# Optimization experiments

Hardware: AMD Instinct MI355X
Metric: run time of the kernel (lower is better)

Reference implementation:

```python
import jax, jax.numpy as jnp
import numpy as np

EPS = 1e-10
N_NODES = 100000
OUT_CH = 128
N_EDGES = 625000


def setup_inputs() -> dict:
    key = jax.random.key(0)
    k_emb, k_eidx, k_enorm, k_lw, k_sw = jax.random.split(key, 5)
    emb = jax.random.normal(k_emb, (N_NODES, OUT_CH), dtype=jnp.float32) * 0.02
    edge_index = jax.random.randint(k_eidx, (2, N_EDGES), 0, N_NODES, dtype=jnp.int64)
    edge_norm = jax.random.uniform(k_enorm, (N_EDGES,), dtype=jnp.float32)
    scale = 1.0 / np.sqrt(OUT_CH)
    loc_w = jax.random.normal(k_lw, (OUT_CH, OUT_CH), dtype=jnp.float32) * scale
    loc_b = jnp.zeros((OUT_CH,), dtype=jnp.float32)
    std_w = jax.random.normal(k_sw, (OUT_CH, OUT_CH), dtype=jnp.float32) * scale
    std_b = jnp.zeros((OUT_CH,), dtype=jnp.float32)
    return {"emb": emb, "edge_index": edge_index, "edge_norm": edge_norm,
            "loc_w": loc_w, "loc_b": loc_b, "std_w": std_w, "std_b": std_b}


def reference(emb, edge_index, edge_norm, loc_w, loc_b, std_w, std_b):
    """GraphEncoder (GraphConv gather-scale-scatter + Linear loc/std) followed by
    GraphDecoder dot-product logits on the same edge list. Eval mode: z = loc."""
    sidx = edge_index[0]
    tidx = edge_index[1]
    # GraphConv: message = x[sidx] * enorm ; scatter_add into target nodes
    message = emb[sidx] * edge_norm[:, None]               # [E, C]
    ptr = jax.ops.segment_sum(message, tidx, num_segments=emb.shape[0])  # [N, C]
    # Encoder heads (torch Linear: x @ W.T + b)
    loc = ptr @ loc_w.T + loc_b                            # [N, C]
    std = jax.nn.softplus(ptr @ std_w.T + std_b) + EPS     # [N, C]
    z = loc  # eval-mode embedding
    # GraphDecoder: Bernoulli logits per edge
    logits = jnp.sum(z[sidx] * z[tidx], axis=1)            # [E]
    return loc, std, logits
```

## Files before the change

### kernel.cpp

```cpp
#include <hip/hip_runtime.h>

#define N_NODES 100000
#define OUT_CH  128
#define N_EDGES 625000

typedef short short8 __attribute__((ext_vector_type(8)));
typedef float f32x4  __attribute__((ext_vector_type(4)));
typedef float f32x2  __attribute__((ext_vector_type(2)));

__device__ inline short f32_bf16(float f) {
    union { float f; unsigned u; } c{f};
    unsigned r = 0x7FFFu + ((c.u >> 16) & 1u);
    return (short)((c.u + r) >> 16);
}
__device__ inline float bf16_f32(short s) {
    union { unsigned u; float f; } c;
    c.u = ((unsigned)(unsigned short)s) << 16;
    return c.f;
}
__device__ inline unsigned pack_bf16x2(float lo, float hi) {
    return (unsigned)(unsigned short)f32_bf16(lo) |
           ((unsigned)(unsigned short)f32_bf16(hi) << 16);
}
__device__ inline float sp_fast(float x) {
    float e = __expf(-fabsf(x));
    return fmaxf(x, 0.f) + __logf(1.f + e);
}

#if defined(__has_builtin)
#if __has_builtin(__builtin_amdgcn_cvt_pk_f32_fp8) && __has_builtin(__builtin_amdgcn_cvt_pk_fp8_f32)
#define HWFP8 1
#endif
#endif
#ifndef HWFP8
#define HWFP8 0
#endif

__device__ inline unsigned f32_fp8_manual(float f) {
    union { float fl; unsigned u; } c{f};
    unsigned s = (c.u >> 31) << 7;
    float af = fabsf(f);
    if (!(af < 448.f)) return s | 0x7E;
    if (af < 0.015625f) {
        unsigned q = (unsigned)__float2int_rn(af * 512.f);
        return s | q;
    }
    unsigned u = c.u;
    u += 0x7FFFF + ((u >> 20) & 1);
    int e = (int)((u >> 23) & 255) - 127;
    if (e > 8) return s | 0x7E;
    return s | (((unsigned)(e + 7)) << 3) | ((u >> 20) & 7);
}
__device__ inline float fp8_f32_manual(unsigned b) {
    unsigned s = (b >> 7) & 1, e = (b >> 3) & 15, m = b & 7;
    if (e) { union { unsigned u; float f; } c{(s << 31) | ((e + 120) << 23) | (m << 20)}; return c.f; }
    float v = (float)m * 0.001953125f;
    return s ? -v : v;
}

template <bool HI>
__device__ inline f32x2 fp8x2_f32(unsigned v) {
#if HWFP8
    return __builtin_amdgcn_cvt_pk_f32_fp8((int)v, HI);
#else
    unsigned sh = HI ? 16 : 0;
    f32x2 r;
    r.x = fp8_f32_manual((v >> sh) & 0xff);
    r.y = fp8_f32_manual((v >> (sh + 8)) & 0xff);
    return r;
#endif
}
template <bool HI>
__device__ inline unsigned fp8_pack2(float a, float b, unsigned old) {
#if HWFP8
    return (unsigned)__builtin_amdgcn_cvt_pk_fp8_f32(a, b, (int)old, HI);
#else
    unsigned v = f32_fp8_manual(a) | (f32_fp8_manual(b) << 8);
    return HI ? ((old & 0x0000ffffu) | (v << 16)) : ((old & 0xffff0000u) | v);
#endif
}

#define NBB 16
#define NBE 6250
#define NBH 2442
__global__ void prep_all(const float* __restrict__ lw, const float* __restrict__ sw,
                         short8* __restrict__ B, const float4* __restrict__ emb,
                         uint2* __restrict__ embf8, const int* __restrict__ ei,
                         int* __restrict__ counts, int use_fp8) {
    int bid = blockIdx.x, tid = threadIdx.x;
    if (bid < NBB) {
        int g = bid * 256 + tid;
        int lane = g & 63, nt = (g >> 6) & 15, ks = g >> 10;
        int c = nt * 16 + (lane & 15);
        int k = ks * 32 + (lane >> 4) * 8;
        const float* src = (c < OUT_CH) ? (lw + c * OUT_CH + k)
                                        : (sw + (c - OUT_CH) * OUT_CH + k);
        short8 o;
#pragma unroll
        for (int j = 0; j < 8; ++j) o[j] = f32_bf16(src[j]);
        B[(ks * 16 + nt) * 64 + lane] = o;
    } else if (bid < NBB + NBE) {
        if (!use_fp8) return;
        int i = (bid - NBB) * 256 + tid;
        float4 a = emb[2 * i], b = emb[2 * i + 1];
        unsigned lo = fp8_pack2<false>(a.x * 64.f, a.y * 64.f, 0u);
        lo = fp8_pack2<true>(a.z * 64.f, a.w * 64.f, lo);
        unsigned hi = fp8_pack2<false>(b.x * 64.f, b.y * 64.f, 0u);
        hi = fp8_pack2<true>(b.z * 64.f, b.w * 64.f, hi);
        uint2 o; o.x = lo; o.y = hi;
        embf8[i] = o;
    } else {
        int e = (bid - NBB - NBE) * 256 + tid;
        if (e < N_EDGES) atomicAdd(&counts[ei[N_EDGES + e]], 1);
    }
}

__global__ void scan1_k(const int* __restrict__ counts, int* __restrict__ offsets,
                        int* __restrict__ partials, int* __restrict__ cursors) {
    __shared__ int wsum[16];
    int tid = threadIdx.x, lane = tid & 63, wid = tid >> 6;
    int e = blockIdx.x * 1024 + tid;
    int v = (e < N_NODES) ? counts[e] : 0;
    int incl = v;
#pragma unroll
    for (int d = 1; d < 64; d <<= 1) {
        int t = __shfl_up(incl, d);
        if (lane >= d) incl += t;
    }
    if (lane == 63) wsum[wid] = incl;
    __syncthreads();
    if (wid == 0) {
        int w = (lane < 16) ? wsum[lane] : 0;
        int wi = w;
#pragma unroll
        for (int d = 1; d < 16; d <<= 1) {
            int t = __shfl_up(wi, d);
            if (lane >= d) wi += t;
        }
        if (lane < 16) wsum[lane] = wi - w;
        if (lane == 15) partials[blockIdx.x] = wi;
    }
    __syncthreads();
    int excl = incl - v + wsum[wid];
    if (e < N_NODES) { offsets[e] = excl; cursors[e] = excl; }
}

__global__ void scan2_k(int* __restrict__ partials, int nb) {
    int lane = threadIdx.x;
    int i0 = 2 * lane, i1 = 2 * lane + 1;
    int v0 = (i0 < nb) ? partials[i0] : 0;
    int v1 = (i1 < nb) ? partials[i1] : 0;
    int s = v0 + v1;
    int incl = s;
#pragma unroll
    for (int d = 1; d < 64; d <<= 1) {
        int t = __shfl_up(incl, d);
        if (lane >= d) incl += t;
    }
    int excl = incl - s;
    if (i0 < nb) partials[i0] = excl;
    if (i1 < nb) partials[i1] = excl + v0;
}

__global__ void reorder_k(const int* __restrict__ ei, const float* __restrict__ en,
                          const int* __restrict__ partials, int* __restrict__ cursors,
                          int2* __restrict__ pairs, int2* __restrict__ et, float nscale) {
    int e = blockIdx.x * blockDim.x + threadIdx.x;
    if (e >= N_EDGES) return;
    int t = ei[N_EDGES + e];
    int pos = partials[t >> 10] + atomicAdd(&cursors[t], 1);
    int2 p; p.x = ei[e]; p.y = __float_as_int(en[e] * nscale);
    pairs[pos] = p;
    int2 q; q.x = e; q.y = t;
    et[pos] = q;
}

__global__ void gather_fp8_k(const unsigned short* __restrict__ embf8,
                             const int* __restrict__ offsets,
                             const int* __restrict__ partials,
                             const int2* __restrict__ pairs,
                             unsigned* __restrict__ ptrb) {
    int g = blockIdx.x * blockDim.x + threadIdx.x;
    int node = __builtin_amdgcn_readfirstlane(g >> 6);
    int lane = threadIdx.x & 63;
    if (node >= N_NODES) return;
    int beg = offsets[node] + partials[node >> 10];
    int end = (node == N_NODES - 1) ? N_EDGES
              : offsets[node + 1] + partials[(node + 1) >> 10];
    float ax = 0.f, ay = 0.f;
    int j = beg;
    for (; j + 4 <= end; j += 4) {
        int2 p0 = pairs[j], p1 = pairs[j + 1], p2 = pairs[j + 2], p3 = pairs[j + 3];
        unsigned v0 = embf8[(size_t)p0.x * 64 + lane];
        unsigned v1 = embf8[(size_t)p1.x * 64 + lane];
        unsigned v2 = embf8[(size_t)p2.x * 64 + lane];
        unsigned v3 = embf8[(size_t)p3.x * 64 + lane];
        float n0f = __int_as_float(p0.y), n1f = __int_as_float(p1.y);
        float n2f = __int_as_float(p2.y), n3f = __int_as_float(p3.y);
        f32x2 d0 = fp8x2_f32<false>(v0), d1 = fp8x2_f32<false>(v1);
        f32x2 d2 = fp8x2_f32<false>(v2), d3 = fp8x2_f32<false>(v3);
        ax += d0.x * n0f + d1.x * n1f + d2.x * n2f + d3.x * n3f;
        ay += d0.y * n0f + d1.y * n1f + d2.y * n2f + d3.y * n3f;
    }
    for (; j < end; ++j) {
        int2 p = pairs[j];
        float nm = __int_as_float(p.y);
        f32x2 d = fp8x2_f32<false>(embf8[(size_t)p.x * 64 + lane]);
        ax += d.x * nm; ay += d.y * nm;
    }
    ptrb[(size_t)node * 64 + lane] = pack_bf16x2(ax, ay);
}

__global__ void gather_f32_k(const float* __restrict__ emb,
                             const int* __restrict__ offsets,
                             const int* __restrict__ partials,
                             const int2* __restrict__ pairs,
                             unsigned* __restrict__ ptrb) {
    int g = blockIdx.x * blockDim.x + threadIdx.x;
    int node = __builtin_amdgcn_readfirstlane(g >> 6);
    int lane = threadIdx.x & 63;
    if (node >= N_NODES) return;
    int beg = offsets[node] + partials[node >> 10];
    int end = (node == N_NODES - 1) ? N_EDGES
              : offsets[node + 1] + partials[(node + 1) >> 10];
    float ax = 0.f, ay = 0.f;
    const float2* base = (const float2*)emb;
    int j = beg;
    for (; j + 4 <= end; j += 4) {
        int2 p0 = pairs[j], p1 = pairs[j + 1], p2 = pairs[j + 2], p3 = pairs[j + 3];
        float2 v0 = base[(size_t)p0.x * 64 + lane];
        float2 v1 = base[(size_t)p1.x * 64 + lane];
        float2 v2 = base[(size_t)p2.x * 64 + lane];
        float2 v3 = base[(size_t)p3.x * 64 + lane];
        float n0f = __int_as_float(p0.y), n1f = __int_as_float(p1.y);
        float n2f = __int_as_float(p2.y), n3f = __int_as_float(p3.y);
        ax += v0.x * n0f + v1.x * n1f + v2.x * n2f + v3.x * n3f;
        ay += v0.y * n0f + v1.y * n1f + v2.y * n2f + v3.y * n3f;
    }
    for (; j < end; ++j) {
        int2 p = pairs[j];
        float nm = __int_as_float(p.y);
        float2 v = base[(size_t)p.x * 64 + lane];
        ax += v.x * nm; ay += v.y * nm;
    }
    ptrb[(size_t)node * 64 + lane] = pack_bf16x2(ax, ay);
}

__global__ __launch_bounds__(256) void gemm_k(const short* __restrict__ P,
                                              float* __restrict__ out,
                                              const short8* __restrict__ B,
                                              const float* __restrict__ lb,
                                              const float* __restrict__ sb,
                                              unsigned* __restrict__ zf8, int write_z) {
    int tid = threadIdx.x;
    int wave = tid >> 6, lane = tid & 63;
    int n0 = (blockIdx.x * 4 + wave) * 16;
    if (n0 >= N_NODES) return;

    float* loc  = out;
    float* stdo = out + (size_t)N_NODES * OUT_CH;

    int prow = n0 + (lane & 15);
    int kb = (lane >> 4) * 8;

    f32x4 acc[16];
#pragma unroll
    for (int i = 0; i < 16; ++i) acc[i] = (f32x4)(0.f);

#pragma unroll
    for (int ks = 0; ks < 4; ++ks) {
        short8 a = *(const short8*)(P + (size_t)prow * OUT_CH + ks * 32 + kb);
#pragma unroll
        for (int nt = 0; nt < 16; ++nt) {
            short8 w = B[(ks * 16 + nt) * 64 + lane];
            acc[nt] = __builtin_amdgcn_mfma_f32_16x16x32_bf16(w, a, acc[nt], 0, 0, 0);
        }
    }

    int node = n0 + (lane & 15);
    int ch4 = (lane >> 4) * 4;
    float* lrow = loc  + (size_t)node * OUT_CH;
    float* srow = stdo + (size_t)node * OUT_CH;
    unsigned* zrow = zf8 + (size_t)node * 32;

#pragma unroll
    for (int nt = 0; nt < 8; ++nt) {
        int c = nt * 16 + ch4;
        float4 b4 = *(const float4*)(lb + c);
        float4 v;
        v.x = acc[nt][0] + b4.x; v.y = acc[nt][1] + b4.y;
        v.z = acc[nt][2] + b4.z; v.w = acc[nt][3] + b4.w;
        *(float4*)(lrow + c) = v;
        if (write_z) {
            unsigned zp = fp8_pack2<false>(v.x * 16.f, v.y * 16.f, 0u);
            zp = fp8_pack2<true>(v.z * 16.f, v.w * 16.f, zp);
            zrow[c >> 2] = zp;
        }
    }
#pragma unroll
    for (int nt = 8; nt < 16; ++nt) {
        int cc = nt * 16 + ch4 - OUT_CH;
        float4 b4 = *(const float4*)(sb + cc);
        float4 v;
        v.x = sp_fast(acc[nt][0] + b4.x) + 1e-10f;
        v.y = sp_fast(acc[nt][1] + b4.y) + 1e-10f;
        v.z = sp_fast(acc[nt][2] + b4.z) + 1e-10f;
        v.w = sp_fast(acc[nt][3] + b4.w) + 1e-10f;
        *(float4*)(srow + cc) = v;
    }
}

__global__ void logits_fp8_k(const unsigned* __restrict__ zf8,
                             const int2* __restrict__ pairs,
                             const int2* __restrict__ et,
                             float* __restrict__ lg) {
    int idx = blockIdx.x * blockDim.x + threadIdx.x;
    int p = idx >> 4, q = idx & 15;
    if (p >= N_EDGES) return;
    int s = pairs[p].x;
    int2 me = et[p];
    uint2 a = *(const uint2*)(zf8 + (size_t)s * 32 + q * 2);
    uint2 b = *(const uint2*)(zf8 + (size_t)me.y * 32 + q * 2);
    f32x2 a0 = fp8x2_f32<false>(a.x), a1 = fp8x2_f32<true>(a.x);
    f32x2 a2 = fp8x2_f32<false>(a.y), a3 = fp8x2_f32<true>(a.y);
    f32x2 b0 = fp8x2_f32<false>(b.x), b1 = fp8x2_f32<true>(b.x);
    f32x2 b2 = fp8x2_f32<false>(b.y), b3 = fp8x2_f32<true>(b.y);
    float d = a0.x * b0.x + a0.y * b0.y + a1.x * b1.x + a1.y * b1.y
            + a2.x * b2.x + a2.y * b2.y + a3.x * b3.x + a3.y * b3.y;
#pragma unroll
    for (int m = 8; m >= 1; m >>= 1) d += __shfl_xor(d, m);
    if (q == 0) lg[me.x] = d * 0.00390625f;
}

__global__ void logits_f32_k(const float* __restrict__ z, const int* __restrict__ ei,
                             float* __restrict__ lg) {
    int idx = blockIdx.x * blockDim.x + threadIdx.x;
    int e = idx >> 5, q = idx & 31;
    if (e >= N_EDGES) return;
    int s = ei[e], t = ei[N_EDGES + e];
    float4 a = *(const float4*)(z + (size_t)s * OUT_CH + q * 4);
    float4 b = *(const float4*)(z + (size_t)t * OUT_CH + q * 4);
    float d = a.x * b.x + a.y * b.y + a.z * b.z + a.w * b.w;
#pragma unroll
    for (int m = 16; m >= 1; m >>= 1) d += __shfl_xor(d, m);
    if (q == 0) lg[e] = d;
}

extern "C" void kernel_launch(void* const* d_in, const int* in_sizes, int n_in,
                              void* d_out, int out_size, void* d_ws, size_t ws_size,
                              hipStream_t stream) {
    const float* emb = (const float*)d_in[0];
    const int*   ei  = (const int*)d_in[1];
    const float* en  = (const float*)d_in[2];
    const float* lw  = (const float*)d_in[3];
    const float* lb  = (const float*)d_in[4];
    const float* sw  = (const float*)d_in[5];
    const float* sb  = (const float*)d_in[6];
    float* out = (float*)d_out;

    char* ws = (char*)d_ws;
    size_t o = 0;
    short8* B       = (short8*)(ws + o); o += 65536;
    int*    counts  = (int*)(ws + o);    o += 400128;
    int*    offsets = (int*)(ws + o);    o += 400128;
    int*    cursors = (int*)(ws + o);    o += 400128;
    int*    partials= (int*)(ws + o);    o += 1024;
    int2*   pairs   = (int2*)(ws + o);   o += (size_t)N_EDGES * 8;
    int2*   et      = (int2*)(ws + o);   o += (size_t)N_EDGES * 8;
    unsigned* ptrb  = (unsigned*)(ws + o); o += (size_t)N_NODES * OUT_CH * 2;

    unsigned* zf8   = (unsigned*)(ws + o);
    unsigned short* embf8 = (unsigned short*)(ws + o + (size_t)N_NODES * OUT_CH);
    size_t o_end = o + (size_t)N_NODES * OUT_CH * 2;
    int use_fp8 = (o_end <= ws_size) ? 1 : 0;

    hipMemsetAsync(counts, 0, N_NODES * sizeof(int), stream);

    prep_all<<<NBB + NBE + NBH, 256, 0, stream>>>(lw, sw, B, (const float4*)emb,
                                                  (uint2*)embf8, ei, counts, use_fp8);
    scan1_k<<<98, 1024, 0, stream>>>(counts, offsets, partials, cursors);
    scan2_k<<<1, 64, 0, stream>>>(partials, 98);
    reorder_k<<<(N_EDGES + 255) / 256, 256, 0, stream>>>(
        ei, en, partials, cursors, pairs, et, use_fp8 ? 0.015625f : 1.0f);
    if (use_fp8)
        gather_fp8_k<<<(N_NODES * 64 + 255) / 256, 256, 0, stream>>>(
            embf8, offsets, partials, pairs, ptrb);
    else
        gather_f32_k<<<(N_NODES * 64 + 255) / 256, 256, 0, stream>>>(
            emb, offsets, partials, pairs, ptrb);
    gemm_k<<<(N_NODES / 16 + 3) / 4, 256, 0, stream>>>((const short*)ptrb, out, B,
                                                       lb, sb, zf8, use_fp8);
    float* lg = out + (size_t)2 * N_NODES * OUT_CH;
    if (use_fp8)
        logits_fp8_k<<<((size_t)N_EDGES * 16 + 255) / 256, 256, 0, stream>>>(
            zf8, pairs, et, lg);
    else
        logits_f32_k<<<((size_t)N_EDGES * 32 + 255) / 256, 256, 0, stream>>>(out, ei, lg);
}
```

Measured before the change: 192.1 us.

## Merge edge arrays, fuse scan passes, per-thread logits, nontemporal output stores

Packs the separate pairs and edge/target arrays into one 16-byte record per edge, so reorder writes one record and logits reads one. The second scan kernel is folded into scan1 through a last-block-done atomic, which removes a launch. The fp8 logits kernel now gives each thread a whole edge, doing 128-byte vector loads and no shuffle reduction. GEMM and logits outputs use nontemporal stores. Costs: the gather kernel loads 16-byte records where it used 8, and one thread per edge brings less memory parallelism per row.

```diff
diff --git a/kernel.cpp b/kernel.cpp
--- a/kernel.cpp
+++ b/kernel.cpp
@@ -3,6 +3,7 @@
 #define N_NODES 100000
 #define OUT_CH  128
 #define N_EDGES 625000
+#define NB_SCAN 98
 
 typedef short short8 __attribute__((ext_vector_type(8)));
 typedef float f32x4  __attribute__((ext_vector_type(4)));
@@ -13,11 +14,6 @@
     unsigned r = 0x7FFFu + ((c.u >> 16) & 1u);
     return (short)((c.u + r) >> 16);
 }
-__device__ inline float bf16_f32(short s) {
-    union { unsigned u; float f; } c;
-    c.u = ((unsigned)(unsigned short)s) << 16;
-    return c.f;
-}
 __device__ inline unsigned pack_bf16x2(float lo, float hi) {
     return (unsigned)(unsigned short)f32_bf16(lo) |
            ((unsigned)(unsigned short)f32_bf16(hi) << 16);
@@ -26,6 +22,16 @@
     float e = __expf(-fabsf(x));
     return fmaxf(x, 0.f) + __logf(1.f + e);
 }
+
+#if defined(__has_builtin)
+#if __has_builtin(__builtin_nontemporal_store)
+#define NTS(p, v) __builtin_nontemporal_store((v), (p))
+#else
+#define NTS(p, v) (*(p) = (v))
+#endif
+#else
+#define NTS(p, v) (*(p) = (v))
+#endif
 
 #if defined(__has_builtin)
 #if __has_builtin(__builtin_amdgcn_cvt_pk_f32_fp8) && __has_builtin(__builtin_amdgcn_cvt_pk_fp8_f32)
@@ -116,8 +122,10 @@
 }
 
 __global__ void scan1_k(const int* __restrict__ counts, int* __restrict__ offsets,
-                        int* __restrict__ partials, int* __restrict__ cursors) {
+                        int* __restrict__ partials, int* __restrict__ cursors,
+                        int* __restrict__ done) {
     __shared__ int wsum[16];
+    __shared__ int lastFlag;
     int tid = threadIdx.x, lane = tid & 63, wid = tid >> 6;
     int e = blockIdx.x * 1024 + tid;
     int v = (e < N_NODES) ? counts[e] : 0;
@@ -143,42 +151,47 @@
     __syncthreads();
     int excl = incl - v + wsum[wid];
     if (e < N_NODES) { offsets[e] = excl; cursors[e] = excl; }
-}
-
-__global__ void scan2_k(int* __restrict__ partials, int nb) {
-    int lane = threadIdx.x;
-    int i0 = 2 * lane, i1 = 2 * lane + 1;
-    int v0 = (i0 < nb) ? partials[i0] : 0;
-    int v1 = (i1 < nb) ? partials[i1] : 0;
-    int s = v0 + v1;
-    int incl = s;
-#pragma unroll
-    for (int d = 1; d < 64; d <<= 1) {
-        int t = __shfl_up(incl, d);
-        if (lane >= d) incl += t;
-    }
-    int excl = incl - s;
-    if (i0 < nb) partials[i0] = excl;
-    if (i1 < nb) partials[i1] = excl + v0;
+
+    __threadfence();
+    if (tid == 0) lastFlag = (atomicAdd(done, 1) == NB_SCAN - 1) ? 1 : 0;
+    __syncthreads();
+    if (lastFlag && wid == 0) {
+        __threadfence();
+        int i0 = 2 * lane, i1 = 2 * lane + 1;
+        int v0 = (i0 < NB_SCAN) ? atomicAdd(&partials[i0], 0) : 0;
+        int v1 = (i1 < NB_SCAN) ? atomicAdd(&partials[i1], 0) : 0;
+        int s = v0 + v1;
+        int incl2 = s;
+#pragma unroll
+        for (int d = 1; d < 64; d <<= 1) {
+            int t = __shfl_up(incl2, d);
+            if (lane >= d) incl2 += t;
+        }
+        int ex2 = incl2 - s;
+        if (i0 < NB_SCAN) partials[i0] = ex2;
+        if (i1 < NB_SCAN) partials[i1] = ex2 + v0;
+    }
 }
 
 __global__ void reorder_k(const int* __restrict__ ei, const float* __restrict__ en,
                           const int* __restrict__ partials, int* __restrict__ cursors,
-                          int2* __restrict__ pairs, int2* __restrict__ et, float nscale) {
+                          int4* __restrict__ edata, float nscale) {
     int e = blockIdx.x * blockDim.x + threadIdx.x;
     if (e >= N_EDGES) return;
     int t = ei[N_EDGES + e];
     int pos = partials[t >> 10] + atomicAdd(&cursors[t], 1);
-    int2 p; p.x = ei[e]; p.y = __float_as_int(en[e] * nscale);
-    pairs[pos] = p;
-    int2 q; q.x = e; q.y = t;
-    et[pos] = q;
+    int4 d;
+    d.x = ei[e];
+    d.y = __float_as_int(en[e] * nscale);
+    d.z = e;
+    d.w = t;
+    edata[pos] = d;
 }
 
 __global__ void gather_fp8_k(const unsigned short* __restrict__ embf8,
                              const int* __restrict__ offsets,
                              const int* __restrict__ partials,
-                             const int2* __restrict__ pairs,
+                             const int4* __restrict__ edata,
                              unsigned* __restrict__ ptrb) {
     int g = blockIdx.x * blockDim.x + threadIdx.x;
     int node = __builtin_amdgcn_readfirstlane(g >> 6);
@@ -190,7 +203,7 @@
     float ax = 0.f, ay = 0.f;
     int j = beg;
     for (; j + 4 <= end; j += 4) {
-        int2 p0 = pairs[j], p1 = pairs[j + 1], p2 = pairs[j + 2], p3 = pairs[j + 3];
+        int4 p0 = edata[j], p1 = edata[j + 1], p2 = edata[j + 2], p3 = edata[j + 3];
         unsigned v0 = embf8[(size_t)p0.x * 64 + lane];
         unsigned v1 = embf8[(size_t)p1.x * 64 + lane];
         unsigned v2 = embf8[(size_t)p2.x * 64 + lane];
@@ -203,7 +216,7 @@
         ay += d0.y * n0f + d1.y * n1f + d2.y * n2f + d3.y * n3f;
     }
     for (; j < end; ++j) {
-        int2 p = pairs[j];
+        int4 p = edata[j];
         float nm = __int_as_float(p.y);
         f32x2 d = fp8x2_f32<false>(embf8[(size_t)p.x * 64 + lane]);
         ax += d.x * nm; ay += d.y * nm;
@@ -214,7 +227,7 @@
 __global__ void gather_f32_k(const float* __restrict__ emb,
                              const int* __restrict__ offsets,
                              const int* __restrict__ partials,
-                             const int2* __restrict__ pairs,
+                             const int4* __restrict__ edata,
                              unsigned* __restrict__ ptrb) {
     int g = blockIdx.x * blockDim.x + threadIdx.x;
     int node = __builtin_amdgcn_readfirstlane(g >> 6);
@@ -227,7 +240,7 @@
     const float2* base = (const float2*)emb;
     int j = beg;
     for (; j + 4 <= end; j += 4) {
-        int2 p0 = pairs[j], p1 = pairs[j + 1], p2 = pairs[j + 2], p3 = pairs[j + 3];
+        int4 p0 = edata[j], p1 = edata[j + 1], p2 = edata[j + 2], p3 = edata[j + 3];
         float2 v0 = base[(size_t)p0.x * 64 + lane];
         float2 v1 = base[(size_t)p1.x * 64 + lane];
         float2 v2 = base[(size_t)p2.x * 64 + lane];
@@ -238,7 +251,7 @@
         ay += v0.y * n0f + v1.y * n1f + v2.y * n2f + v3.y * n3f;
     }
     for (; j < end; ++j) {
-        int2 p = pairs[j];
+        int4 p = edata[j];
         float nm = __int_as_float(p.y);
         float2 v = base[(size_t)p.x * 64 + lane];
         ax += v.x * nm; ay += v.y * nm;
@@ -287,13 +300,13 @@
     for (int nt = 0; nt < 8; ++nt) {
         int c = nt * 16 + ch4;
         float4 b4 = *(const float4*)(lb + c);
-        float4 v;
-        v.x = acc[nt][0] + b4.x; v.y = acc[nt][1] + b4.y;
-        v.z = acc[nt][2] + b4.z; v.w = acc[nt][3] + b4.w;
-        *(float4*)(lrow + c) = v;
+        f32x4 v;
+        v[0] = acc[nt][0] + b4.x; v[1] = acc[nt][1] + b4.y;
+        v[2] = acc[nt][2] + b4.z; v[3] = acc[nt][3] + b4.w;
+        NTS((f32x4*)(lrow + c), v);
         if (write_z) {
-            unsigned zp = fp8_pack2<false>(v.x * 16.f, v.y * 16.f, 0u);
-            zp = fp8_pack2<true>(v.z * 16.f, v.w * 16.f, zp);
+            unsigned zp = fp8_pack2<false>(v[0] * 16.f, v[1] * 16.f, 0u);
+            zp = fp8_pack2<true>(v[2] * 16.f, v[3] * 16.f, zp);
             zrow[c >> 2] = zp;
         }
     }
@@ -301,35 +314,40 @@
     for (int nt = 8; nt < 16; ++nt) {
         int cc = nt * 16 + ch4 - OUT_CH;
         float4 b4 = *(const float4*)(sb + cc);
-        float4 v;
-        v.x = sp_fast(acc[nt][0] + b4.x) + 1e-10f;
-        v.y = sp_fast(acc[nt][1] + b4.y) + 1e-10f;
-        v.z = sp_fast(acc[nt][2] + b4.z) + 1e-10f;
-        v.w = sp_fast(acc[nt][3] + b4.w) + 1e-10f;
-        *(float4*)(srow + cc) = v;
-    }
-}
-
-__global__ void logits_fp8_k(const unsigned* __restrict__ zf8,
-                             const int2* __restrict__ pairs,
-                             const int2* __restrict__ et,
+        f32x4 v;
+        v[0] = sp_fast(acc[nt][0] + b4.x) + 1e-10f;
+        v[1] = sp_fast(acc[nt][1] + b4.y) + 1e-10f;
+        v[2] = sp_fast(acc[nt][2] + b4.z) + 1e-10f;
+        v[3] = sp_fast(acc[nt][3] + b4.w) + 1e-10f;
+        NTS((f32x4*)(srow + cc), v);
+    }
+}
+
+typedef unsigned u32x4 __attribute__((ext_vector_type(4)));
+__global__ void logits_fp8_k(const u32x4* __restrict__ zf8,
+                             const int4* __restrict__ edata,
                              float* __restrict__ lg) {
-    int idx = blockIdx.x * blockDim.x + threadIdx.x;
-    int p = idx >> 4, q = idx & 15;
+    int p = blockIdx.x * blockDim.x + threadIdx.x;
     if (p >= N_EDGES) return;
-    int s = pairs[p].x;
-    int2 me = et[p];
-    uint2 a = *(const uint2*)(zf8 + (size_t)s * 32 + q * 2);
-    uint2 b = *(const uint2*)(zf8 + (size_t)me.y * 32 + q * 2);
-    f32x2 a0 = fp8x2_f32<false>(a.x), a1 = fp8x2_f32<true>(a.x);
-    f32x2 a2 = fp8x2_f32<false>(a.y), a3 = fp8x2_f32<true>(a.y);
-    f32x2 b0 = fp8x2_f32<false>(b.x), b1 = fp8x2_f32<true>(b.x);
-    f32x2 b2 = fp8x2_f32<false>(b.y), b3 = fp8x2_f32<true>(b.y);
-    float d = a0.x * b0.x + a0.y * b0.y + a1.x * b1.x + a1.y * b1.y
-            + a2.x * b2.x + a2.y * b2.y + a3.x * b3.x + a3.y * b3.y;
-#pragma unroll
-    for (int m = 8; m >= 1; m >>= 1) d += __shfl_xor(d, m);
-    if (q == 0) lg[me.x] = d * 0.00390625f;
+    int4 md = edata[p];
+    const u32x4* sa = zf8 + (size_t)md.x * 8;
+    const u32x4* tb = zf8 + (size_t)md.w * 8;
+    u32x4 A[8], Bv[8];
+#pragma unroll
+    for (int i = 0; i < 8; ++i) A[i] = sa[i];
+#pragma unroll
+    for (int i = 0; i < 8; ++i) Bv[i] = tb[i];
+    float d = 0.f;
+#pragma unroll
+    for (int i = 0; i < 8; ++i) {
+#pragma unroll
+        for (int k = 0; k < 4; ++k) {
+            f32x2 al = fp8x2_f32<false>(A[i][k]), ah = fp8x2_f32<true>(A[i][k]);
+            f32x2 bl = fp8x2_f32<false>(Bv[i][k]), bh = fp8x2_f32<true>(Bv[i][k]);
+            d += al.x * bl.x + al.y * bl.y + ah.x * bh.x + ah.y * bh.y;
+        }
+    }
+    NTS(&lg[md.z], d * 0.00390625f);
 }
 
 __global__ void logits_f32_k(const float* __restrict__ z, const int* __restrict__ ei,
@@ -362,11 +380,11 @@
     size_t o = 0;
     short8* B       = (short8*)(ws + o); o += 65536;
     int*    counts  = (int*)(ws + o);    o += 400128;
+    int*    done    = (int*)((char*)counts + 400000);
     int*    offsets = (int*)(ws + o);    o += 400128;
     int*    cursors = (int*)(ws + o);    o += 400128;
     int*    partials= (int*)(ws + o);    o += 1024;
-    int2*   pairs   = (int2*)(ws + o);   o += (size_t)N_EDGES * 8;
-    int2*   et      = (int2*)(ws + o);   o += (size_t)N_EDGES * 8;
+    int4*   edata   = (int4*)(ws + o);   o += (size_t)N_EDGES * 16;
     unsigned* ptrb  = (unsigned*)(ws + o); o += (size_t)N_NODES * OUT_CH * 2;
 
     unsigned* zf8   = (unsigned*)(ws + o);
@@ -374,26 +392,25 @@
     size_t o_end = o + (size_t)N_NODES * OUT_CH * 2;
     int use_fp8 = (o_end <= ws_size) ? 1 : 0;
 
-    hipMemsetAsync(counts, 0, N_NODES * sizeof(int), stream);
+    hipMemsetAsync(counts, 0, 400128, stream);
 
     prep_all<<<NBB + NBE + NBH, 256, 0, stream>>>(lw, sw, B, (const float4*)emb,
                                                   (uint2*)embf8, ei, counts, use_fp8);
-    scan1_k<<<98, 1024, 0, stream>>>(counts, offsets, partials, cursors);
-    scan2_k<<<1, 64, 0, stream>>>(partials, 98);
+    scan1_k<<<NB_SCAN, 1024, 0, stream>>>(counts, offsets, partials, cursors, done);
     reorder_k<<<(N_EDGES + 255) / 256, 256, 0, stream>>>(
-        ei, en, partials, cursors, pairs, et, use_fp8 ? 0.015625f : 1.0f);
+        ei, en, partials, cursors, edata, use_fp8 ? 0.015625f : 1.0f);
     if (use_fp8)
         gather_fp8_k<<<(N_NODES * 64 + 255) / 256, 256, 0, stream>>>(
-            embf8, offsets, partials, pairs, ptrb);
+            embf8, offsets, partials, edata, ptrb);
     else
         gather_f32_k<<<(N_NODES * 64 + 255) / 256, 256, 0, stream>>>(
-            emb, offsets, partials, pairs, ptrb);
+            emb, offsets, partials, edata, ptrb);
     gemm_k<<<(N_NODES / 16 + 3) / 4, 256, 0, stream>>>((const short*)ptrb, out, B,
                                                        lb, sb, zf8, use_fp8);
     float* lg = out + (size_t)2 * N_NODES * OUT_CH;
     if (use_fp8)
-        logits_fp8_k<<<((size_t)N_EDGES * 16 + 255) / 256, 256, 0, stream>>>(
-            zf8, pairs, et, lg);
+        logits_fp8_k<<<(N_EDGES + 255) / 256, 256, 0, stream>>>(
+            (const u32x4*)zf8, edata, lg);
     else
         logits_f32_k<<<((size_t)N_EDGES * 32 + 255) / 256, 256, 0, stream>>>(out, ei, lg);
 }
```

Result: slower. 211.0 us (+9.8%).
